# Performance work log

Measured on AMD Instinct MI355X. Metric: run time of the kernel, lower is better.

Reference implementation:

```python
import jax, jax.numpy as jnp
import numpy as np

N = 207      # nodes (hardcoded in source)
D = 128      # hid_dim
H = 8        # attention heads
C = D // H   # head dim
L = 4        # num_layers
B = 16       # batch
NO = 3       # number of orbits
SZ = 69      # orbit size
EPS = 1e-5
SLOPE = 0.2  # GATv2 leaky_relu negative slope


def _cat_matrix():
    # edge category for pair (i,j): off-diag -> pos_i*NO+pos_j, diag -> NO^2+pos_i
    pos = np.arange(N) // SZ
    c = pos[:, None] * NO + pos[None, :]
    np.fill_diagonal(c, NO * NO + pos)
    return c  # [N, N] int


def setup_inputs() -> dict:
    key = jax.random.key(0)
    ks = jax.random.split(key, 16)
    s = 0.05
    rn = lambda k, shape: jax.random.normal(k, shape, jnp.float32) * s
    return {
        "x": jax.random.normal(ks[0], (B, N, 6), jnp.float32),
        "cat": jnp.asarray(_cat_matrix(), jnp.int32),          # [N,N] edge categories
        "emb": rn(ks[1], (NO * NO + NO, D)),                   # edge embedding table
        "in1_W": rn(ks[2], (D, 6)), "in1_b": jnp.zeros((D,)),
        "ln1_g": jnp.ones((D,)), "ln1_b": jnp.zeros((D,)),
        "in2_W": rn(ks[3], (D, D)), "in2_b": jnp.zeros((D,)),
        "ln2_g": jnp.ones((D,)), "ln2_b": jnp.zeros((D,)),
        "Wl": rn(ks[4], (L, D, D)), "bl": jnp.zeros((L, D)),   # GATv2 lin_l (source)
        "Wr": rn(ks[5], (L, D, D)), "br": jnp.zeros((L, D)),   # GATv2 lin_r (target)
        "We": rn(ks[6], (L, D, D)),                            # GATv2 lin_edge (no bias)
        "att": rn(ks[7], (L, H, C)),                           # attention vector
        "cb": jnp.zeros((L, D)),                               # conv output bias
        "pW": rn(ks[8], (L, D, D)), "pb": jnp.zeros((L, D)),   # projection layers
        "lng": jnp.ones((L, D)), "lnb": jnp.zeros((L, D)),     # per-layer LayerNorm
        "oW": rn(ks[9], (2, D)), "ob": jnp.zeros((2,)),        # output layer
    }


def _ln(x, g, b):
    m = x.mean(-1, keepdims=True)
    v = ((x - m) ** 2).mean(-1, keepdims=True)
    return (x - m) * jax.lax.rsqrt(v + EPS) * g + b


def _fwd(cat, x, emb, in1_W, in1_b, ln1_g, ln1_b, in2_W, in2_b, ln2_g, ln2_b,
         Wl, bl, Wr, br, We, att, cb, pW, pb, lng, lnb, oW, ob):
    # input MLP: Linear -> LN -> ReLU -> Linear -> LN
    h = jax.nn.relu(_ln(x @ in1_W.T + in1_b, ln1_g, ln1_b))
    h = _ln(h @ in2_W.T + in2_b, ln2_g, ln2_b)                 # [B,N,D]
    e_all = emb[cat]                                           # [N,N,D] per-edge embedding
    for l in range(L):
        h_prev = h
        gs = (h @ Wl[l].T + bl[l]).reshape(B, N, H, C)         # source transform
        gd = (h @ Wr[l].T + br[l]).reshape(B, N, H, C)         # target transform
        ee = (e_all @ We[l].T).reshape(N, N, H, C)             # edge transform
        # per-edge GATv2 score: edge (i -> j), i source, j target
        z = jax.nn.leaky_relu(gs[:, :, None] + gd[:, None, :] + ee[None], SLOPE)  # [B,i,j,H,C]
        a = jnp.einsum('bijhc,hc->bijh', z, att[l])
        a = jax.nn.softmax(a, axis=1)                          # softmax over sources per target
        o = jnp.einsum('bijh,bihc->bjhc', a, gs).reshape(B, N, D) + cb[l]
        h = h_prev + jax.nn.relu(_ln(o @ pW[l].T + pb[l], lng[l], lnb[l]))
    return h @ oW.T + ob                                       # [B,N,2]


def reference(x, cat, emb, in1_W, in1_b, ln1_g, ln1_b, in2_W, in2_b, ln2_g, ln2_b,
              Wl, bl, Wr, br, We, att, cb, pW, pb, lng, lnb, oW, ob):
    return _fwd(cat, x, emb, in1_W, in1_b, ln1_g, ln1_b, in2_W, in2_b, ln2_g, ln2_b,
                Wl, bl, Wr, br, We, att, cb, pW, pb, lng, lnb, oW, ob)
```

## Files before the change

kernel.cpp:

```cpp
#include <hip/hip_runtime.h>
#include <hip/hip_bf16.h>

#define NN 207
#define DD 128
#define LL 4
#define BB 16
#define ROWS (BB*NN)
#define RB 8
#define LBLK (ROWS/RB)
#define EPSV 1e-5f
#define SLOPE 0.2f
#define GT4B (32*208*4)

template<bool BF>
__device__ __forceinline__ float ldin(const void* p, int i) {
    if (BF) {
        unsigned short u = ((const unsigned short*)p)[i];
        return __uint_as_float(((unsigned)u) << 16);
    } else {
        return ((const float*)p)[i];
    }
}

template<bool BF>
__device__ __forceinline__ void ldw32(const void* W, int base, float* w) {
    if (BF) {
        const uint4* p = (const uint4*)((const unsigned short*)W + base);
#pragma unroll
        for (int q = 0; q < 4; q++) {
            uint4 u = p[q];
            w[q*8+0] = __uint_as_float(u.x << 16);
            w[q*8+1] = __uint_as_float(u.x & 0xFFFF0000u);
            w[q*8+2] = __uint_as_float(u.y << 16);
            w[q*8+3] = __uint_as_float(u.y & 0xFFFF0000u);
            w[q*8+4] = __uint_as_float(u.z << 16);
            w[q*8+5] = __uint_as_float(u.z & 0xFFFF0000u);
            w[q*8+6] = __uint_as_float(u.w << 16);
            w[q*8+7] = __uint_as_float(u.w & 0xFFFF0000u);
        }
    } else {
        const float4* p = (const float4*)((const float*)W + base);
#pragma unroll
        for (int q = 0; q < 8; q++) {
            float4 u = p[q];
            w[q*4+0] = u.x; w[q*4+1] = u.y; w[q*4+2] = u.z; w[q*4+3] = u.w;
        }
    }
}

template<bool BF>
__device__ __forceinline__ float rowdot(const void* W, int rowbase, const float* sh) {
    float acc = 0.f;
    if (BF) {
        const uint4* p = (const uint4*)((const unsigned short*)W + rowbase);
#pragma unroll
        for (int q = 0; q < DD / 8; q++) {
            uint4 u = p[q];
            const float* s = sh + q * 8;
            acc += __uint_as_float(u.x << 16)        * s[0];
            acc += __uint_as_float(u.x & 0xFFFF0000u) * s[1];
            acc += __uint_as_float(u.y << 16)        * s[2];
            acc += __uint_as_float(u.y & 0xFFFF0000u) * s[3];
            acc += __uint_as_float(u.z << 16)        * s[4];
            acc += __uint_as_float(u.z & 0xFFFF0000u) * s[5];
            acc += __uint_as_float(u.w << 16)        * s[6];
            acc += __uint_as_float(u.w & 0xFFFF0000u) * s[7];
        }
    } else {
        const float4* p = (const float4*)((const float*)W + rowbase);
#pragma unroll
        for (int q = 0; q < DD / 4; q++) {
            float4 u = p[q];
            const float* s = sh + q * 4;
            acc += u.x * s[0]; acc += u.y * s[1]; acc += u.z * s[2]; acc += u.w * s[3];
        }
    }
    return acc;
}

__global__ void k_detect(const unsigned int* g1bits, int* flag) {
    *flag = (g1bits[0] == 0x3F803F80u) ? 1 : 0;
}

template<bool BF>
__device__ void et_body(float* sh, const void* emb, const void* We, float* et) {
    int l = blockIdx.x / 12, c = blockIdx.x % 12, d = threadIdx.x;
    sh[d] = ldin<BF>(emb, c * DD + d);
    __syncthreads();
    et[(l * 12 + c) * DD + d] = rowdot<BF>(We, l * DD * DD + d * DD, sh);
}
__global__ void k_et(const int* flag, const void* emb, const void* We, float* et) {
    __shared__ __align__(16) float smem[DD];
    if (*flag) et_body<true>(smem, emb, We, et);
    else       et_body<false>(smem, emb, We, et);
}

template<bool BF>
__device__ void mlp1_body(float* smem, const void* x, const void* W1, const void* b1,
                          const void* g1, const void* bv1, float* tmp) {
    float* s_x   = smem;
    float* so    = s_x + 48;
    float* stats = so + RB * 132;
    int r0 = blockIdx.x * RB, d = threadIdx.x;
    if (d < RB * 6) s_x[d] = ldin<BF>(x, r0 * 6 + d);
    __syncthreads();
    float w6[6];
#pragma unroll
    for (int k = 0; k < 6; k++) w6[k] = ldin<BF>(W1, d * 6 + k);
    float b0 = ldin<BF>(b1, d);
#pragma unroll
    for (int rr = 0; rr < RB; rr++) {
        float a = b0;
#pragma unroll
        for (int k = 0; k < 6; k++) a += w6[k] * s_x[rr * 6 + k];
        so[rr * 132 + d] = a;
    }
    __syncthreads();
    int rr2 = d >> 4, l16 = d & 15;
    float s = 0.f, sq = 0.f;
#pragma unroll
    for (int k = 0; k < 8; k++) { float v = so[rr2 * 132 + l16 + 16 * k]; s += v; sq += v * v; }
    s += __shfl_xor(s, 1); s += __shfl_xor(s, 2); s += __shfl_xor(s, 4); s += __shfl_xor(s, 8);
    sq += __shfl_xor(sq, 1); sq += __shfl_xor(sq, 2); sq += __shfl_xor(sq, 4); sq += __shfl_xor(sq, 8);
    if (l16 == 0) {
        float mean = s * (1.f / DD);
        float var = sq * (1.f / DD) - mean * mean;
        stats[rr2 * 2] = mean; stats[rr2 * 2 + 1] = rsqrtf(var + EPSV);
    }
    __syncthreads();
    float gv = ldin<BF>(g1, d), bb = ldin<BF>(bv1, d);
#pragma unroll
    for (int rr = 0; rr < RB; rr++) {
        float v = (so[rr * 132 + d] - stats[rr * 2]) * stats[rr * 2 + 1] * gv + bb;
        tmp[(r0 + rr) * DD + d] = fmaxf(v, 0.f);
    }
}
__global__ void k_mlp1(const int* flag, const void* x, const void* W1, const void* b1,
                       const void* g1, const void* bv1, float* tmp) {
    __shared__ __align__(16) float smem[48 + RB * 132 + RB * 2];
    if (*flag) mlp1_body<true>(smem, x, W1, b1, g1, bv1, tmp);
    else       mlp1_body<false>(smem, x, W1, b1, g1, bv1, tmp);
}

template<bool BF>
__device__ void lin_body(float* smem, int epi, const float* in, const void* W, int wOff,
                         const void* bias, const void* g, const void* bv, int dOff,
                         float* h) {
    float* sh    = smem;
    float* so    = sh + RB * DD;
    float* stats = so + RB * 132;
    int r0 = blockIdx.x * RB;
    int t = threadIdx.x, d = t & 127, half = t >> 7;
    float4* sh4 = (float4*)sh;
    const float4* iin = (const float4*)(in + r0 * DD);
    sh4[t] = iin[t];
    __syncthreads();
    float acc[4];
    float b0 = ldin<BF>(bias, dOff + d);
#pragma unroll
    for (int rr = 0; rr < 4; rr++) acc[rr] = b0;
#pragma unroll
    for (int c = 0; c < 4; c++) {
        float w[32];
        ldw32<BF>(W, wOff + d * DD + c * 32, w);
#pragma unroll
        for (int rr = 0; rr < 4; rr++) {
            const float* s = sh + (half * 4 + rr) * DD + c * 32;
            float a = acc[rr];
#pragma unroll
            for (int k = 0; k < 32; k++) a += s[k] * w[k];
            acc[rr] = a;
        }
    }
#pragma unroll
    for (int rr = 0; rr < 4; rr++) so[(half * 4 + rr) * 132 + d] = acc[rr];
    __syncthreads();
    int rr2 = t >> 5, l32 = t & 31;
    float s = 0.f, sq = 0.f;
#pragma unroll
    for (int k = 0; k < 4; k++) { float v = so[rr2 * 132 + l32 + 32 * k]; s += v; sq += v * v; }
    s += __shfl_xor(s, 1); s += __shfl_xor(s, 2); s += __shfl_xor(s, 4);
    s += __shfl_xor(s, 8); s += __shfl_xor(s, 16);
    sq += __shfl_xor(sq, 1); sq += __shfl_xor(sq, 2); sq += __shfl_xor(sq, 4);
    sq += __shfl_xor(sq, 8); sq += __shfl_xor(sq, 16);
    if (l32 == 0) {
        float mean = s * (1.f / DD);
        float var = sq * (1.f / DD) - mean * mean;
        stats[rr2 * 2] = mean; stats[rr2 * 2 + 1] = rsqrtf(var + EPSV);
    }
    __syncthreads();
    float gv = ldin<BF>(g, dOff + d), bb = ldin<BF>(bv, dOff + d);
#pragma unroll
    for (int rr = 0; rr < 4; rr++) {
        int row = half * 4 + rr;
        float v = (so[row * 132 + d] - stats[row * 2]) * stats[row * 2 + 1] * gv + bb;
        int rg = r0 + row;
        if (epi) h[(size_t)rg * DD + d] += fmaxf(v, 0.f);
        else     h[(size_t)rg * DD + d] = v;
    }
}
__global__ void k_lin(const int* flag, int epi, const float* in, const void* W, int wOff,
                      const void* bias, const void* g, const void* bv, int dOff, float* h) {
    __shared__ __align__(16) float smem[RB * DD + RB * 132 + RB * 2];
    if (*flag) lin_body<true>(smem, epi, in, W, wOff, bias, g, bv, dOff, h);
    else       lin_body<false>(smem, epi, in, W, wOff, bias, g, bv, dOff, h);
}

template<bool BF>
__device__ void gsgd_body(float* sh, int l, const float* h, const void* Wl, const void* bl,
                          const void* Wr, const void* br, float* gs, float* gd) {
    int r0 = blockIdx.x * RB;
    int t = threadIdx.x, d = t & 127, mat = t >> 7;
    float4* sh4 = (float4*)sh;
    const float4* hin = (const float4*)(h + r0 * DD);
    sh4[t] = hin[t];
    __syncthreads();
    const void* W  = mat ? Wr : Wl;
    const void* bv = mat ? br : bl;
    float acc[RB];
    float b0 = ldin<BF>(bv, l * DD + d);
#pragma unroll
    for (int rr = 0; rr < RB; rr++) acc[rr] = b0;
#pragma unroll
    for (int c = 0; c < 4; c++) {
        float w[32];
        ldw32<BF>(W, l * DD * DD + d * DD + c * 32, w);
#pragma unroll
        for (int rr = 0; rr < RB; rr++) {
            const float* s = sh + rr * DD + c * 32;
            float a = acc[rr];
#pragma unroll
            for (int k = 0; k < 32; k++) a += s[k] * w[k];
            acc[rr] = a;
        }
    }
    float* outp = mat ? gd : gs;
#pragma unroll
    for (int rr = 0; rr < RB; rr++) outp[(size_t)(r0 + rr) * DD + d] = acc[rr];
}
__global__ void k_gsgd(const int* flag, int l, const float* h, const void* Wl, const void* bl,
                       const void* Wr, const void* br, float* gs, float* gd) {
    __shared__ __align__(16) float smem[RB * DD];
    if (*flag) gsgd_body<true>(smem, l, h, Wl, bl, Wr, br, gs, gd);
    else       gsgd_body<false>(smem, l, h, Wl, bl, Wr, br, gs, gd);
}

__global__ void __launch_bounds__(256, 4) k_trans(const float* gs, float* gs_t4) {
    __shared__ __align__(16) float sb[RB * 132];
    int q = blockIdx.x;
    int batch = q / 26, pr = q - batch * 26;
    int brow0 = pr * 8;
    int nrows = NN - brow0; if (nrows > RB) nrows = RB;
    int t = threadIdx.x;
    int srow = t >> 5, se = t & 31;
    int cr = srow < nrows ? srow : nrows - 1;
    ((float4*)(sb + srow * 132))[se] =
        ((const float4*)(gs + (size_t)(batch * NN + brow0 + cr) * DD))[se];
    __syncthreads();
    int d4 = t >> 3, ii = t & 7;
    if (ii < nrows) {
        float4 v;
        v.x = sb[ii * 132 + d4 * 4 + 0];
        v.y = sb[ii * 132 + d4 * 4 + 1];
        v.z = sb[ii * 132 + d4 * 4 + 2];
        v.w = sb[ii * 132 + d4 * 4 + 3];
        ((float4*)(gs_t4 + (size_t)batch * GT4B))[d4 * 208 + brow0 + ii] = v;
    }
}

#define ATTN_SMEM (1584*2 + 128 + 1696*2 + 16 + 1024 + 416)
template<bool BF>
__device__ void attn_body(float* smem, int l, const float* gs, const float* gd, const float* et,
                          const float* gs_t4, const int* cat, const void* att, const void* cb,
                          float* o) {
    float* s_ge1 = smem;
    float* s_ge2 = s_ge1 + 1584;
    float* s_att = s_ge2 + 1584;
    float* s_pe1 = s_att + 128;
    float* s_pe2 = s_pe1 + 1696;
    float* s_inv = s_pe2 + 1696;
    float* s_prt = s_inv + 16;
    int*   s_cat1 = (int*)(s_prt + 1024);
    int*   s_cat2 = s_cat1 + 208;
    int p = blockIdx.x;
    int kk = (p & 7) * 208 + (p >> 3);
    int b = kk / 104, k = kk - b * 104;
    int j1 = k, j2 = k + 104;
    bool has2 = (k < 103);
    int r1 = b * NN + j1, r2 = b * NN + j2;
    int t = threadIdx.x;
    if (t < DD) s_att[t] = ldin<BF>(att, l * DD + t);
    for (int idx = t; idx < NN; idx += 256) {
        s_cat1[idx] = cat[idx * NN + j1];
        s_cat2[idx] = has2 ? cat[idx * NN + j2] : 0;
    }
    for (int idx = t; idx < 12 * DD; idx += 256) {
        int c = idx >> 7, kd = idx & 127;
        float ev = et[l * 12 * DD + idx];
        s_ge1[c * 132 + kd] = ev + gd[(size_t)r1 * DD + kd];
        s_ge2[c * 132 + kd] = has2 ? (ev + gd[(size_t)r2 * DD + kd]) : 0.f;
    }
    __syncthreads();
    if (t < NN) {
        const float4* gt  = ((const float4*)(gs_t4 + (size_t)b * GT4B)) + t;
        const float4* ge1 = (const float4*)(s_ge1 + s_cat1[t] * 132);
        const float4* ge2 = (const float4*)(s_ge2 + s_cat2[t] * 132);
        const float4* at  = (const float4*)s_att;
        float a1[8], a2[8];
#pragma unroll
        for (int hh = 0; hh < 8; hh++) { a1[hh] = 0.f; a2[hh] = 0.f; }
#pragma unroll
        for (int q = 0; q < 32; q++) {
            float4 g4 = gt[q * 208];
            float4 A  = at[q];
            float4 e1 = ge1[q];
            float z0 = g4.x + e1.x, z1 = g4.y + e1.y, z2 = g4.z + e1.z, z3 = g4.w + e1.w;
            z0 = fmaxf(z0, SLOPE * z0); z1 = fmaxf(z1, SLOPE * z1);
            z2 = fmaxf(z2, SLOPE * z2); z3 = fmaxf(z3, SLOPE * z3);
            a1[q >> 2] += A.x * z0 + A.y * z1 + A.z * z2 + A.w * z3;
            float4 e2 = ge2[q];
            float y0 = g4.x + e2.x, y1 = g4.y + e2.y, y2 = g4.z + e2.z, y3 = g4.w + e2.w;
            y0 = fmaxf(y0, SLOPE * y0); y1 = fmaxf(y1, SLOPE * y1);
            y2 = fmaxf(y2, SLOPE * y2); y3 = fmaxf(y3, SLOPE * y3);
            a2[q >> 2] += A.x * y0 + A.y * y1 + A.z * y2 + A.w * y3;
        }
#pragma unroll
        for (int hh = 0; hh < 8; hh++) {
            s_pe1[hh * 212 + t] = a1[hh];
            s_pe2[hh * 212 + t] = a2[hh];
        }
    }
    __syncthreads();
    {
        int g = t >> 4, l16 = t & 15;
        float* pe = (g < 8) ? s_pe1 : s_pe2;
        int hh = g & 7;
        float vals[13]; float mx = -1e30f;
#pragma unroll
        for (int kq = 0; kq < 13; kq++) {
            int i = l16 + 16 * kq;
            vals[kq] = (i < NN) ? pe[hh * 212 + i] : -1e30f;
            mx = fmaxf(mx, vals[kq]);
        }
        mx = fmaxf(mx, __shfl_xor(mx, 1)); mx = fmaxf(mx, __shfl_xor(mx, 2));
        mx = fmaxf(mx, __shfl_xor(mx, 4)); mx = fmaxf(mx, __shfl_xor(mx, 8));
        float sum = 0.f;
#pragma unroll
        for (int kq = 0; kq < 13; kq++) {
            int i = l16 + 16 * kq;
            float e = (i < NN) ? __expf(vals[kq] - mx) : 0.f;
            if (i < 208) pe[hh * 212 + i] = e;
            sum += e;
        }
        sum += __shfl_xor(sum, 1); sum += __shfl_xor(sum, 2);
        sum += __shfl_xor(sum, 4); sum += __shfl_xor(sum, 8);
        if (l16 == 0) s_inv[g] = 1.f / sum;
    }
    __syncthreads();
    float4 p1, p2;
    int d4 = t & 31, sg = t >> 5;
    {
        int hh = d4 >> 2;
        const float4* g4p = ((const float4*)(gs + (size_t)b * NN * DD)) + d4;
        const float* e1 = s_pe1 + hh * 212;
        const float* e2 = s_pe2 + hh * 212;
        int i0 = sg * 26;
        int i1 = i0 + 26; if (i1 > NN) i1 = NN;
        p1.x = p1.y = p1.z = p1.w = 0.f;
        p2.x = p2.y = p2.z = p2.w = 0.f;
        for (int i = i0; i < i1; i++) {
            float4 g4 = g4p[i * 32];
            float w1 = e1[i], w2 = e2[i];
            p1.x = fmaf(w1, g4.x, p1.x); p1.y = fmaf(w1, g4.y, p1.y);
            p1.z = fmaf(w1, g4.z, p1.z); p1.w = fmaf(w1, g4.w, p1.w);
            p2.x = fmaf(w2, g4.x, p2.x); p2.y = fmaf(w2, g4.y, p2.y);
            p2.z = fmaf(w2, g4.z, p2.z); p2.w = fmaf(w2, g4.w, p2.w);
        }
    }
    ((float4*)s_prt)[sg * 32 + d4] = p1;
    __syncthreads();
    if (t < 128) {
        float sum = 0.f;
#pragma unroll
        for (int s = 0; s < 8; s++) sum += s_prt[s * 128 + t];
        o[(size_t)r1 * DD + t] = sum * s_inv[t >> 4] + ldin<BF>(cb, l * DD + t);
    }
    __syncthreads();
    ((float4*)s_prt)[sg * 32 + d4] = p2;
    __syncthreads();
    if (t < 128 && has2) {
        float sum = 0.f;
#pragma unroll
        for (int s = 0; s < 8; s++) sum += s_prt[s * 128 + t];
        o[(size_t)r2 * DD + t] = sum * s_inv[8 + (t >> 4)] + ldin<BF>(cb, l * DD + t);
    }
}
__global__ void __launch_bounds__(256, 4)
k_attn(const int* flag, int l, const float* gs, const float* gd, const float* et,
       const float* gs_t4, const int* cat, const void* att, const void* cb,
       float* o) {
    __shared__ __align__(16) float smem[ATTN_SMEM];
    if (*flag) attn_body<true>(smem, l, gs, gd, et, gs_t4, cat, att, cb, o);
    else       attn_body<false>(smem, l, gs, gd, et, gs_t4, cat, att, cb, o);
}

__device__ __forceinline__ void blk_red2(float& a, float& b, float* red) {
#pragma unroll
    for (int m = 32; m; m >>= 1) { a += __shfl_xor(a, m); b += __shfl_xor(b, m); }
    int wid = threadIdx.x >> 6;
    if ((threadIdx.x & 63) == 0) { red[wid * 2] = a; red[wid * 2 + 1] = b; }
    __syncthreads();
    a = red[0] + red[2];
    b = red[1] + red[3];
    __syncthreads();
}
template<bool BF>
__device__ void out_body(float* red, const float* h, const void* oW, const void* ob, void* out) {
    int r = blockIdx.x, d = threadIdx.x;
    float hv = h[(size_t)r * DD + d];
    float p0 = hv * ldin<BF>(oW, d);
    float p1 = hv * ldin<BF>(oW, DD + d);
    blk_red2(p0, p1, red);
    if (d < 2) {
        float v = (d == 0 ? p0 : p1) + ldin<BF>(ob, d);
        if (BF) ((__hip_bfloat16*)out)[r * 2 + d] = __float2bfloat16(v);
        else    ((float*)out)[r * 2 + d] = v;
    }
}
__global__ void k_out(const int* flag, const float* h, const void* oW, const void* ob, void* out) {
    __shared__ float red[4];
    if (*flag) out_body<true>(red, h, oW, ob, out);
    else       out_body<false>(red, h, oW, ob, out);
}

extern "C" void kernel_launch(void* const* d_in, const int* in_sizes, int n_in,
                              void* d_out, int out_size, void* d_ws, size_t ws_size,
                              hipStream_t stream) {
    const void* x     = d_in[0];
    const int*  cat   = (const int*)d_in[1];
    const void* emb   = d_in[2];
    const void* in1W  = d_in[3];
    const void* in1b  = d_in[4];
    const void* ln1g  = d_in[5];
    const void* ln1b  = d_in[6];
    const void* in2W  = d_in[7];
    const void* in2b  = d_in[8];
    const void* ln2g  = d_in[9];
    const void* ln2b  = d_in[10];
    const void* Wl    = d_in[11];
    const void* bl    = d_in[12];
    const void* Wr    = d_in[13];
    const void* br    = d_in[14];
    const void* We    = d_in[15];
    const void* att   = d_in[16];
    const void* cb    = d_in[17];
    const void* pW    = d_in[18];
    const void* pb    = d_in[19];
    const void* lng   = d_in[20];
    const void* lnb   = d_in[21];
    const void* oW    = d_in[22];
    const void* ob    = d_in[23];

    float* ws  = (float*)d_ws;
    int*  flag = (int*)d_ws;
    float* h     = ws + 16;
    float* gs    = h    + ROWS * DD;
    float* gd    = gs   + ROWS * DD;
    float* o     = gd   + ROWS * DD;
    float* et    = o    + ROWS * DD;
    float* gs_t4 = et   + LL * 12 * DD;
    float* tmp   = gs;

    k_detect<<<1, 1, 0, stream>>>((const unsigned int*)ln1g, flag);
    k_et<<<LL * 12, DD, 0, stream>>>(flag, emb, We, et);
    k_mlp1<<<LBLK, DD, 0, stream>>>(flag, x, in1W, in1b, ln1g, ln1b, tmp);
    k_lin<<<LBLK, 256, 0, stream>>>(flag, 0, tmp, in2W, 0, in2b, ln2g, ln2b, 0, h);
    for (int l = 0; l < LL; l++) {
        k_gsgd<<<LBLK, 256, 0, stream>>>(flag, l, h, Wl, bl, Wr, br, gs, gd);
        k_trans<<<BB * 26, 256, 0, stream>>>(gs, gs_t4);
        k_attn<<<BB * 104, 256, 0, stream>>>(flag, l, gs, gd, et, gs_t4, cat, att, cb, o);
        k_lin<<<LBLK, 256, 0, stream>>>(flag, 1, o, pW, l * DD * DD, pb, lng, lnb, l * DD, h);
    }
    k_out<<<ROWS, DD, 0, stream>>>(flag, h, oW, ob, d_out);
}
```

Baseline: 366.2 us.

## Fuse projection, next-layer source/target transforms and transpose into one kernel

The projection+LayerNorm+residual kernel now keeps the updated h rows in shared memory and immediately computes the next layer's gs/gd linear transforms and writes the transposed gs_t4 layout. This replaces three launches per layer (lin, gsgd, trans) with one and avoids re-reading h and gs from global memory. The cost is larger shared memory per block and extra serial work per block, which may reduce occupancy.

```diff
diff --git a/kernel.cpp b/kernel.cpp
--- a/kernel.cpp
+++ b/kernel.cpp
@@ -142,18 +142,21 @@
     else       mlp1_body<false>(smem, x, W1, b1, g1, bv1, tmp);
 }
 
-template<bool BF>
-__device__ void lin_body(float* smem, int epi, const float* in, const void* W, int wOff,
-                         const void* bias, const void* g, const void* bv, int dOff,
-                         float* h) {
+#define LING_SMEM (RB*DD + RB*132 + 16 + RB*128)
+template<bool BF>
+__device__ void linG_body(float* smem, int epi, int hasNext,
+                          const float* in, const void* W, int wOff,
+                          const void* bias, const void* g, const void* bv, int dOff,
+                          const void* Wl, const void* bl, const void* Wr, const void* br,
+                          int nwOff, int nbOff,
+                          float* h, float* gs, float* gd, float* gs_t4) {
     float* sh    = smem;
     float* so    = sh + RB * DD;
     float* stats = so + RB * 132;
+    float* s_gs  = stats + 16;
     int r0 = blockIdx.x * RB;
     int t = threadIdx.x, d = t & 127, half = t >> 7;
-    float4* sh4 = (float4*)sh;
-    const float4* iin = (const float4*)(in + r0 * DD);
-    sh4[t] = iin[t];
+    ((float4*)sh)[t] = ((const float4*)(in + (size_t)r0 * DD))[t];
     __syncthreads();
     float acc[4];
     float b0 = ldin<BF>(bias, dOff + d);
@@ -193,79 +196,71 @@
 #pragma unroll
     for (int rr = 0; rr < 4; rr++) {
         int row = half * 4 + rr;
+        int rg = r0 + row;
         float v = (so[row * 132 + d] - stats[row * 2]) * stats[row * 2 + 1] * gv + bb;
-        int rg = r0 + row;
-        if (epi) h[(size_t)rg * DD + d] += fmaxf(v, 0.f);
-        else     h[(size_t)rg * DD + d] = v;
-    }
-}
-__global__ void k_lin(const int* flag, int epi, const float* in, const void* W, int wOff,
-                      const void* bias, const void* g, const void* bv, int dOff, float* h) {
-    __shared__ __align__(16) float smem[RB * DD + RB * 132 + RB * 2];
-    if (*flag) lin_body<true>(smem, epi, in, W, wOff, bias, g, bv, dOff, h);
-    else       lin_body<false>(smem, epi, in, W, wOff, bias, g, bv, dOff, h);
-}
-
-template<bool BF>
-__device__ void gsgd_body(float* sh, int l, const float* h, const void* Wl, const void* bl,
-                          const void* Wr, const void* br, float* gs, float* gd) {
-    int r0 = blockIdx.x * RB;
-    int t = threadIdx.x, d = t & 127, mat = t >> 7;
-    float4* sh4 = (float4*)sh;
-    const float4* hin = (const float4*)(h + r0 * DD);
-    sh4[t] = hin[t];
-    __syncthreads();
-    const void* W  = mat ? Wr : Wl;
-    const void* bv = mat ? br : bl;
-    float acc[RB];
-    float b0 = ldin<BF>(bv, l * DD + d);
-#pragma unroll
-    for (int rr = 0; rr < RB; rr++) acc[rr] = b0;
-#pragma unroll
-    for (int c = 0; c < 4; c++) {
-        float w[32];
-        ldw32<BF>(W, l * DD * DD + d * DD + c * 32, w);
-#pragma unroll
-        for (int rr = 0; rr < RB; rr++) {
-            const float* s = sh + rr * DD + c * 32;
-            float a = acc[rr];
-#pragma unroll
-            for (int k = 0; k < 32; k++) a += s[k] * w[k];
-            acc[rr] = a;
-        }
-    }
-    float* outp = mat ? gd : gs;
-#pragma unroll
-    for (int rr = 0; rr < RB; rr++) outp[(size_t)(r0 + rr) * DD + d] = acc[rr];
-}
-__global__ void k_gsgd(const int* flag, int l, const float* h, const void* Wl, const void* bl,
-                       const void* Wr, const void* br, float* gs, float* gd) {
-    __shared__ __align__(16) float smem[RB * DD];
-    if (*flag) gsgd_body<true>(smem, l, h, Wl, bl, Wr, br, gs, gd);
-    else       gsgd_body<false>(smem, l, h, Wl, bl, Wr, br, gs, gd);
-}
-
-__global__ void __launch_bounds__(256, 4) k_trans(const float* gs, float* gs_t4) {
-    __shared__ __align__(16) float sb[RB * 132];
-    int q = blockIdx.x;
-    int batch = q / 26, pr = q - batch * 26;
-    int brow0 = pr * 8;
-    int nrows = NN - brow0; if (nrows > RB) nrows = RB;
-    int t = threadIdx.x;
-    int srow = t >> 5, se = t & 31;
-    int cr = srow < nrows ? srow : nrows - 1;
-    ((float4*)(sb + srow * 132))[se] =
-        ((const float4*)(gs + (size_t)(batch * NN + brow0 + cr) * DD))[se];
-    __syncthreads();
-    int d4 = t >> 3, ii = t & 7;
-    if (ii < nrows) {
+        float hn;
+        if (epi) hn = h[(size_t)rg * DD + d] + fmaxf(v, 0.f);
+        else     hn = v;
+        h[(size_t)rg * DD + d] = hn;
+        sh[row * DD + d] = hn;
+    }
+    __syncthreads();
+    if (!hasNext) return;
+    {
+        const void* Wm = half ? Wr : Wl;
+        const void* bm = half ? br : bl;
+        float acc2[RB];
+        float bn = ldin<BF>(bm, nbOff + d);
+#pragma unroll
+        for (int rr = 0; rr < RB; rr++) acc2[rr] = bn;
+#pragma unroll
+        for (int c = 0; c < 4; c++) {
+            float w[32];
+            ldw32<BF>(Wm, nwOff + d * DD + c * 32, w);
+#pragma unroll
+            for (int rr = 0; rr < RB; rr++) {
+                const float* s = sh + rr * DD + c * 32;
+                float a = acc2[rr];
+#pragma unroll
+                for (int k = 0; k < 32; k++) a += s[k] * w[k];
+                acc2[rr] = a;
+            }
+        }
+        if (half) {
+#pragma unroll
+            for (int rr = 0; rr < RB; rr++) gd[(size_t)(r0 + rr) * DD + d] = acc2[rr];
+        } else {
+#pragma unroll
+            for (int rr = 0; rr < RB; rr++) {
+                gs[(size_t)(r0 + rr) * DD + d] = acc2[rr];
+                s_gs[rr * DD + d] = acc2[rr];
+            }
+        }
+    }
+    __syncthreads();
+    {
+        int d4 = t >> 3, iL = t & 7;
+        int rg = r0 + iL;
+        int bb2 = rg / NN, ii = rg - bb2 * NN;
         float4 v;
-        v.x = sb[ii * 132 + d4 * 4 + 0];
-        v.y = sb[ii * 132 + d4 * 4 + 1];
-        v.z = sb[ii * 132 + d4 * 4 + 2];
-        v.w = sb[ii * 132 + d4 * 4 + 3];
-        ((float4*)(gs_t4 + (size_t)batch * GT4B))[d4 * 208 + brow0 + ii] = v;
-    }
+        v.x = s_gs[iL * DD + d4 * 4 + 0];
+        v.y = s_gs[iL * DD + d4 * 4 + 1];
+        v.z = s_gs[iL * DD + d4 * 4 + 2];
+        v.w = s_gs[iL * DD + d4 * 4 + 3];
+        ((float4*)(gs_t4 + (size_t)bb2 * GT4B))[d4 * 208 + ii] = v;
+    }
+}
+__global__ void k_linG(const int* flag, int epi, int hasNext,
+                       const float* in, const void* W, int wOff,
+                       const void* bias, const void* g, const void* bv, int dOff,
+                       const void* Wl, const void* bl, const void* Wr, const void* br,
+                       int nwOff, int nbOff,
+                       float* h, float* gs, float* gd, float* gs_t4) {
+    __shared__ __align__(16) float smem[LING_SMEM];
+    if (*flag) linG_body<true>(smem, epi, hasNext, in, W, wOff, bias, g, bv, dOff,
+                               Wl, bl, Wr, br, nwOff, nbOff, h, gs, gd, gs_t4);
+    else       linG_body<false>(smem, epi, hasNext, in, W, wOff, bias, g, bv, dOff,
+                                Wl, bl, Wr, br, nwOff, nbOff, h, gs, gd, gs_t4);
 }
 
 #define ATTN_SMEM (1584*2 + 128 + 1696*2 + 16 + 1024 + 416)
@@ -474,12 +469,14 @@
     k_detect<<<1, 1, 0, stream>>>((const unsigned int*)ln1g, flag);
     k_et<<<LL * 12, DD, 0, stream>>>(flag, emb, We, et);
     k_mlp1<<<LBLK, DD, 0, stream>>>(flag, x, in1W, in1b, ln1g, ln1b, tmp);
-    k_lin<<<LBLK, 256, 0, stream>>>(flag, 0, tmp, in2W, 0, in2b, ln2g, ln2b, 0, h);
+    k_linG<<<LBLK, 256, 0, stream>>>(flag, 0, 1, tmp, in2W, 0, in2b, ln2g, ln2b, 0,
+                                     Wl, bl, Wr, br, 0, 0, h, gs, gd, gs_t4);
     for (int l = 0; l < LL; l++) {
-        k_gsgd<<<LBLK, 256, 0, stream>>>(flag, l, h, Wl, bl, Wr, br, gs, gd);
-        k_trans<<<BB * 26, 256, 0, stream>>>(gs, gs_t4);
         k_attn<<<BB * 104, 256, 0, stream>>>(flag, l, gs, gd, et, gs_t4, cat, att, cb, o);
-        k_lin<<<LBLK, 256, 0, stream>>>(flag, 1, o, pW, l * DD * DD, pb, lng, lnb, l * DD, h);
+        k_linG<<<LBLK, 256, 0, stream>>>(flag, 1, (l < LL - 1) ? 1 : 0, o,
+                                         pW, l * DD * DD, pb, lng, lnb, l * DD,
+                                         Wl, bl, Wr, br, (l + 1) * DD * DD, (l + 1) * DD,
+                                         h, gs, gd, gs_t4);
     }
     k_out<<<ROWS, DD, 0, stream>>>(flag, h, oW, ob, d_out);
 }
```

After: 349.4 us. 1.05x faster.
